# Kernel optimization log

Hardware: AMD Instinct MI355X
Metric: run time of the kernel (lower is better)

The kernel has to match this reference:

```python
import jax, jax.numpy as jnp
import numpy as np

N, K, F_DIM, D = 50000, 20, 256, 128


def setup_inputs() -> dict:
    key = jax.random.key(0)
    ks = jax.random.split(key, 8)
    s = 0.05  # small init scale for numerical stability
    return {
        "h": jax.random.normal(ks[0], (N, F_DIM), dtype=jnp.float32),
        "aggregate_neighbors": jax.random.randint(ks[1], (N, K), 0, N),
        "W_past": jax.random.normal(ks[2], (F_DIM, D), dtype=jnp.float32) * s,
        "W": jax.random.normal(ks[3], (2 * D, D), dtype=jnp.float32) * s,
        "W_ih": jax.random.normal(ks[4], (4 * D, D), dtype=jnp.float32) * s,
        "W_hh": jax.random.normal(ks[5], (4 * D, D), dtype=jnp.float32) * s,
        "b_ih": jax.random.normal(ks[6], (4 * D,), dtype=jnp.float32) * s,
        "b_hh": jax.random.normal(ks[7], (4 * D,), dtype=jnp.float32) * s,
    }


def _lstm(seq, W_ih, W_hh, b_ih, b_hh):
    # seq: (N, K, D) batch_first single-layer LSTM; returns final (h_n, c_n), each (N, D)
    n, _, d = seq.shape

    def step(carry, x_t):
        h_t, c_t = carry
        gates = x_t @ W_ih.T + b_ih + h_t @ W_hh.T + b_hh  # (N, 4D)
        i, f, g, o = jnp.split(gates, 4, axis=-1)
        c = jax.nn.sigmoid(f) * c_t + jax.nn.sigmoid(i) * jnp.tanh(g)
        h_new = jax.nn.sigmoid(o) * jnp.tanh(c)
        return (h_new, c), None

    init = (jnp.zeros((n, d), seq.dtype), jnp.zeros((n, d), seq.dtype))
    (h_n, c_n), _ = jax.lax.scan(step, init, jnp.swapaxes(seq, 0, 1))
    return h_n, c_n


def reference(h, aggregate_neighbors, W_past, W, W_ih, W_hh, b_ih, b_hh):
    hp = h @ W_past                      # (N, D) projected features
    seq = hp[aggregate_neighbors]        # (N, K, D) per-node neighbor gather
    h_n, c_n = _lstm(seq, W_ih, W_hh, b_ih, b_hh)
    neigh = jnp.concatenate([hp, h_n], axis=1)  # (N, 2D)
    out = jax.nn.elu(neigh @ W)          # (N, D)
    return out, h_n, c_n
```

## Files before the change

### kernel.cpp

```cpp
#include <hip/hip_runtime.h>

#define NN 50000
#define KSEQ 20
#define HN_OFF 6400000
#define CN_OFF 12800000

using short8 = __attribute__((ext_vector_type(8))) short;
using f32x4  = __attribute__((ext_vector_type(4))) float;

__device__ __forceinline__ unsigned short f2bf(float f) {
    unsigned int u = __float_as_uint(f);
    return (unsigned short)((u + 0x7FFFu + ((u >> 16) & 1u)) >> 16);
}
__device__ __forceinline__ float exp2x(float x) { float r; asm("v_exp_f32 %0, %1" : "=v"(r) : "v"(x)); return r; }
__device__ __forceinline__ float rcpx(float x)  { float r; asm("v_rcp_f32 %0, %1" : "=v"(r) : "v"(x)); return r; }

#define L2E 1.4426950408889634f
__device__ __forceinline__ float sigp(float y)  { return rcpx(1.f + exp2x(y)); }
__device__ __forceinline__ float tanhp(float y) { return fmaf(-2.f, rcpx(1.f + exp2x(y)), 1.f); }

__global__ void prep_kernel(const float* __restrict__ Wp, const float* __restrict__ W,
                            const float* __restrict__ Wih, const float* __restrict__ Whh,
                            const float* __restrict__ bih, const float* __restrict__ bhh,
                            unsigned short* __restrict__ Wih_b, unsigned short* __restrict__ Whh_b,
                            unsigned short* __restrict__ Wpt, unsigned short* __restrict__ Wtt,
                            float* __restrict__ bsum) {
    int tid = blockIdx.x * blockDim.x + threadIdx.x;
    if (tid < 65536) {
        float sc = ((tid >> 14) == 2) ? (2.f * L2E) : (-L2E);
        Wih_b[tid] = f2bf(Wih[tid] * sc); return;
    }
    tid -= 65536;
    if (tid < 65536) {
        float sc = ((tid >> 14) == 2) ? (2.f * L2E) : (-L2E);
        Whh_b[tid] = f2bf(Whh[tid] * sc); return;
    }
    tid -= 65536;
    if (tid < 32768) { int j = tid >> 8, k = tid & 255; Wpt[tid] = f2bf(Wp[k * 128 + j]); return; }
    tid -= 32768;
    if (tid < 32768) { int j = tid >> 8, k = tid & 255; Wtt[tid] = f2bf(W[k * 128 + j]); return; }
    tid -= 32768;
    if (tid < 512) {
        float sc = ((tid >> 7) == 2) ? (2.f * L2E) : (-L2E);
        bsum[tid] = (bih[tid] + bhh[tid]) * sc;
    }
}

__global__ __launch_bounds__(512, 2) void hp_g_kernel(const float* __restrict__ h,
                                                      const unsigned short* __restrict__ Wpt,
                                                      const unsigned short* __restrict__ Wih_b,
                                                      const float* __restrict__ bsum,
                                                      unsigned short* __restrict__ hp_bf,
                                                      unsigned short* __restrict__ G) {
    __shared__ __align__(16) unsigned char smem[24576];
    const int tid = threadIdx.x;
    const int w = tid >> 6, l = tid & 63;
    const int l15 = l & 15, lq = l >> 4;
    const int base = blockIdx.x * 32;
    const int colj = w * 16 + l15;

#pragma unroll
    for (int i = 0; i < 4; ++i) {
        int chunk = tid + 512 * i;
        int row = chunk >> 6, kc = chunk & 63;
        int grow = base + row;
        float4 v = make_float4(0.f, 0.f, 0.f, 0.f);
        if (grow < NN) v = *(const float4*)(h + (size_t)grow * 256 + kc * 4);
        ushort4 bv = make_ushort4(f2bf(v.x), f2bf(v.y), f2bf(v.z), f2bf(v.w));
        int off = (row * 512 + kc * 8) ^ ((row & 7) << 4);
        *(ushort4*)(smem + off) = bv;
    }
    __syncthreads();

    short8 bf[8];
#pragma unroll
    for (int kt = 0; kt < 8; ++kt)
        bf[kt] = *(const short8*)((const unsigned char*)Wpt + colj * 512 + kt * 64 + lq * 16);

    f32x4 acc[2];
    acc[0] = (f32x4){0.f, 0.f, 0.f, 0.f};
    acc[1] = acc[0];
#pragma unroll
    for (int kt = 0; kt < 8; ++kt) {
#pragma unroll
        for (int rt = 0; rt < 2; ++rt) {
            int arow = rt * 16 + l15;
            int off = (arow * 512 + kt * 64 + lq * 16) ^ ((arow & 7) << 4);
            short8 a = *(const short8*)(smem + off);
            acc[rt] = __builtin_amdgcn_mfma_f32_16x16x32_bf16(a, bf[kt], acc[rt], 0, 0, 0);
        }
    }
#pragma unroll
    for (int rt = 0; rt < 2; ++rt)
#pragma unroll
        for (int r = 0; r < 4; ++r) {
            int row = rt * 16 + lq * 4 + r;
            int grow = base + row;
            unsigned short hb = f2bf(acc[rt][r]);
            if (grow < NN) hp_bf[(size_t)grow * 128 + colj] = hb;
            *(unsigned short*)(smem + 16384 + ((row * 256 + colj * 2) ^ ((row & 7) << 4))) = hb;
        }
    __syncthreads();

    short8 bw4[4][4];
    float bi[4];
#pragma unroll
    for (int g = 0; g < 4; ++g) {
#pragma unroll
        for (int kt = 0; kt < 4; ++kt)
            bw4[g][kt] = *(const short8*)((const unsigned char*)Wih_b + (g * 128 + colj) * 256 + kt * 64 + lq * 16);
        bi[g] = bsum[g * 128 + colj];
    }
    const int off0 = (l15 * 256 + lq * 16) ^ ((l15 & 7) << 4);

    f32x4 ag[4][2];
#pragma unroll
    for (int g = 0; g < 4; ++g) { ag[g][0] = (f32x4){bi[g], bi[g], bi[g], bi[g]}; ag[g][1] = ag[g][0]; }
#pragma unroll
    for (int kt = 0; kt < 4; ++kt)
#pragma unroll
        for (int rt = 0; rt < 2; ++rt) {
            short8 a = *(const short8*)(smem + 16384 + rt * 4096 + (off0 ^ (kt << 6)));
#pragma unroll
            for (int g = 0; g < 4; ++g)
                ag[g][rt] = __builtin_amdgcn_mfma_f32_16x16x32_bf16(a, bw4[g][kt], ag[g][rt], 0, 0, 0);
        }
#pragma unroll
    for (int rt = 0; rt < 2; ++rt)
#pragma unroll
        for (int e = 0; e < 4; ++e) {
            int grow = base + rt * 16 + lq * 4 + e;
            if (grow < NN) {
                ushort4 pk = make_ushort4(f2bf(ag[0][rt][e]), f2bf(ag[1][rt][e]),
                                          f2bf(ag[2][rt][e]), f2bf(ag[3][rt][e]));
                *(ushort4*)(G + (size_t)grow * 512 + colj * 4) = pk;
            }
        }
}

template<int RP>
__device__ __forceinline__ void lstm_step(unsigned char* lds, int t,
    uint2 (&gx)[2][4], const short8 (&bw)[4][4], f32x4& cst,
    const unsigned char* Gp, const unsigned cb,
    const int off0, const int colj, const int lq, const int hwb, const int hswz,
    const int base, float* __restrict__ out)
{
    constexpr int NP = RP ^ 1;
    f32x4 acc[4];
#pragma unroll
    for (int e = 0; e < 4; ++e) {
        uint2 u = gx[RP][e];
        acc[0][e] = __uint_as_float(u.x << 16);
        acc[1][e] = __uint_as_float(u.x & 0xFFFF0000u);
        acc[2][e] = __uint_as_float(u.y << 16);
        acc[3][e] = __uint_as_float(u.y & 0xFFFF0000u);
    }
    if (t > 0) {
        __builtin_amdgcn_s_setprio(1);
#pragma unroll
        for (int kt = 0; kt < 4; ++kt) {
            short8 a = *(const short8*)(lds + RP * 4096 + (off0 ^ (kt << 6)));
#pragma unroll
            for (int g = 0; g < 4; ++g)
                acc[g] = __builtin_amdgcn_mfma_f32_16x16x32_bf16(a, bw[g][kt], acc[g], 0, 0, 0);
        }
        __builtin_amdgcn_s_setprio(0);
    }
    if (t <= 17) {
#pragma unroll
        for (int e = 0; e < 4; ++e) {
            int idx = *(const int*)(lds + 12288 + (lq * 4 + e) * 80 + (t + 2) * 4);
            gx[RP][e] = *(const uint2*)(Gp + (((unsigned)idx << 10) + cb));
        }
    }
#pragma unroll
    for (int e = 0; e < 4; ++e) {
        float c = fmaf(sigp(acc[1][e]), cst[e], sigp(acc[0][e]) * tanhp(acc[2][e]));
        cst[e] = c;
        float hv = sigp(acc[3][e]) * tanhp((2.f * L2E) * c);
        unsigned pk;
        asm("v_cvt_pk_bf16_f32 %0, %1, %2" : "=v"(pk) : "v"(hv), "v"(hv));
        *(unsigned short*)(lds + NP * 4096 + ((hwb + e * 256) ^ (hswz ^ (e << 4)))) = (unsigned short)pk;
        if (t == KSEQ - 1) {
            int grow = base + lq * 4 + e;
            out[HN_OFF + (size_t)grow * 128 + colj] = hv;
            out[CN_OFF + (size_t)grow * 128 + colj] = c;
        }
    }
    __syncthreads();
}

__global__ __launch_bounds__(512, 4) void lstm_kernel(const unsigned short* __restrict__ hp_bf,
                                                      const int* __restrict__ agg,
                                                      const unsigned short* __restrict__ G,
                                                      const unsigned short* __restrict__ Whh_b,
                                                      const unsigned short* __restrict__ Wtt,
                                                      float* __restrict__ out) {
    __shared__ __align__(16) unsigned char lds[14336];
    const int tid = threadIdx.x;
    const int w = tid >> 6, l = tid & 63;
    const int l15 = l & 15, lq = l >> 4;
    const int base = blockIdx.x * 16;
    const int colj = w * 16 + l15;

    if (tid < 256) {
        int row = tid >> 4, c = tid & 15;
        uint4 v = *(const uint4*)((const unsigned char*)hp_bf + (size_t)(base + row) * 256 + c * 16);
        *(uint4*)(lds + 8192 + ((row * 256 + c * 16) ^ ((row & 7) << 4))) = v;
    }
    if (tid < 320) {
        *(int*)(lds + 12288 + tid * 4) = agg[(size_t)base * KSEQ + tid];
    }

    short8 bw[4][4];
#pragma unroll
    for (int g = 0; g < 4; ++g)
#pragma unroll
        for (int kt = 0; kt < 4; ++kt)
            bw[g][kt] = *(const short8*)((const unsigned char*)Whh_b + (g * 128 + colj) * 256 + kt * 64 + lq * 16);

    const int off0 = (l15 * 256 + lq * 16) ^ ((l15 & 7) << 4);
    const int hwb = lq * 1024 + colj * 2;
    const int hswz = (lq & 1) << 6;
    const unsigned char* Gp = (const unsigned char*)G;
    const unsigned cb = (unsigned)colj * 8;

    f32x4 cst = (f32x4){0.f, 0.f, 0.f, 0.f};
    __syncthreads();

    uint2 gx[2][4];
#pragma unroll
    for (int tp = 0; tp < 2; ++tp)
#pragma unroll
        for (int e = 0; e < 4; ++e) {
            int idx = *(const int*)(lds + 12288 + (lq * 4 + e) * 80 + tp * 4);
            gx[tp][e] = *(const uint2*)(Gp + (((unsigned)idx << 10) + cb));
        }

#pragma unroll 1
    for (int tt = 0; tt < KSEQ; tt += 2) {
        lstm_step<0>(lds, tt,     gx, bw, cst, Gp, cb, off0, colj, lq, hwb, hswz, base, out);
        lstm_step<1>(lds, tt + 1, gx, bw, cst, Gp, cb, off0, colj, lq, hwb, hswz, base, out);
    }

    short8 bo[8];
#pragma unroll
    for (int kt = 0; kt < 8; ++kt)
        bo[kt] = *(const short8*)((const unsigned char*)Wtt + colj * 512 + kt * 64 + lq * 16);

    f32x4 a2 = (f32x4){0.f, 0.f, 0.f, 0.f};
#pragma unroll
    for (int kt = 0; kt < 4; ++kt) {
        short8 a = *(const short8*)(lds + 8192 + (off0 ^ (kt << 6)));
        a2 = __builtin_amdgcn_mfma_f32_16x16x32_bf16(a, bo[kt], a2, 0, 0, 0);
    }
#pragma unroll
    for (int kt = 0; kt < 4; ++kt) {
        short8 a = *(const short8*)(lds + (off0 ^ (kt << 6)));
        a2 = __builtin_amdgcn_mfma_f32_16x16x32_bf16(a, bo[kt + 4], a2, 0, 0, 0);
    }
#pragma unroll
    for (int e = 0; e < 4; ++e) {
        int grow = base + lq * 4 + e;
        float v = a2[e];
        out[(size_t)grow * 128 + colj] = (v > 0.f) ? v : (exp2x(L2E * v) - 1.f);
    }
}

extern "C" void kernel_launch(void* const* d_in, const int* in_sizes, int n_in,
                              void* d_out, int out_size, void* d_ws, size_t ws_size,
                              hipStream_t stream) {
    (void)in_sizes; (void)n_in; (void)out_size; (void)ws_size;
    const float* h   = (const float*)d_in[0];
    const int*   agg = (const int*)d_in[1];
    const float* Wp  = (const float*)d_in[2];
    const float* W   = (const float*)d_in[3];
    const float* Wih = (const float*)d_in[4];
    const float* Whh = (const float*)d_in[5];
    const float* bih = (const float*)d_in[6];
    const float* bhh = (const float*)d_in[7];
    float* out = (float*)d_out;

    unsigned short* hp_bf = (unsigned short*)d_ws;
    unsigned short* G     = hp_bf + 6400000;
    unsigned short* Wih_b = G + 25600000;
    unsigned short* Whh_b = Wih_b + 65536;
    unsigned short* Wpt   = Whh_b + 65536;
    unsigned short* Wtt   = Wpt + 32768;
    float*          bsum  = (float*)(Wtt + 32768);

    prep_kernel<<<771, 256, 0, stream>>>(Wp, W, Wih, Whh, bih, bhh, Wih_b, Whh_b, Wpt, Wtt, bsum);
    hp_g_kernel<<<1563, 512, 0, stream>>>(h, Wpt, Wih_b, bsum, hp_bf, G);
    lstm_kernel<<<3125, 512, 0, stream>>>(hp_bf, agg, G, Whh_b, Wtt, out);
}
```

Measured before the change: 300.0 us.

## Single-buffer gate prefetch, transpose index slab, fuse sigmoid/tanh reciprocals

New measurement: 283.4 us. -5.5%, faster.

```diff
diff --git a/kernel.cpp b/kernel.cpp
--- a/kernel.cpp
+++ b/kernel.cpp
@@ -138,23 +138,34 @@
         }
 }
 
+#define SLAB 12288
 template<int RP>
 __device__ __forceinline__ void lstm_step(unsigned char* lds, int t,
-    uint2 (&gx)[2][4], const short8 (&bw)[4][4], f32x4& cst,
+    uint2 (&gx)[4], const short8 (&bw)[4][4], f32x4& cst,
     const unsigned char* Gp, const unsigned cb,
     const int off0, const int colj, const int lq, const int hwb, const int hswz,
     const int base, float* __restrict__ out)
 {
     constexpr int NP = RP ^ 1;
+    int4 idx4;
+    if (t < KSEQ - 1)
+        idx4 = *(const int4*)(lds + SLAB + (t + 1) * 64 + lq * 16);
+
     f32x4 acc[4];
 #pragma unroll
     for (int e = 0; e < 4; ++e) {
-        uint2 u = gx[RP][e];
+        uint2 u = gx[e];
         acc[0][e] = __uint_as_float(u.x << 16);
         acc[1][e] = __uint_as_float(u.x & 0xFFFF0000u);
         acc[2][e] = __uint_as_float(u.y << 16);
         acc[3][e] = __uint_as_float(u.y & 0xFFFF0000u);
     }
+    if (t < KSEQ - 1) {
+        gx[0] = *(const uint2*)(Gp + (((unsigned)idx4.x << 10) + cb));
+        gx[1] = *(const uint2*)(Gp + (((unsigned)idx4.y << 10) + cb));
+        gx[2] = *(const uint2*)(Gp + (((unsigned)idx4.z << 10) + cb));
+        gx[3] = *(const uint2*)(Gp + (((unsigned)idx4.w << 10) + cb));
+    }
     if (t > 0) {
         __builtin_amdgcn_s_setprio(1);
 #pragma unroll
@@ -166,18 +177,17 @@
         }
         __builtin_amdgcn_s_setprio(0);
     }
-    if (t <= 17) {
-#pragma unroll
-        for (int e = 0; e < 4; ++e) {
-            int idx = *(const int*)(lds + 12288 + (lq * 4 + e) * 80 + (t + 2) * 4);
-            gx[RP][e] = *(const uint2*)(Gp + (((unsigned)idx << 10) + cb));
-        }
-    }
 #pragma unroll
     for (int e = 0; e < 4; ++e) {
-        float c = fmaf(sigp(acc[1][e]), cst[e], sigp(acc[0][e]) * tanhp(acc[2][e]));
+        float Ai = 1.f + exp2x(acc[0][e]);
+        float Af = 1.f + exp2x(acc[1][e]);
+        float B  = 1.f + exp2x(acc[2][e]);
+        float AiB = Ai * B;
+        float c = fmaf(cst[e], AiB, Af * (B - 2.f)) * rcpx(Af * AiB);
         cst[e] = c;
-        float hv = sigp(acc[3][e]) * tanhp((2.f * L2E) * c);
+        float C  = 1.f + exp2x((2.f * L2E) * c);
+        float Do = 1.f + exp2x(acc[3][e]);
+        float hv = (C - 2.f) * rcpx(C * Do);
         unsigned pk;
         asm("v_cvt_pk_bf16_f32 %0, %1, %2" : "=v"(pk) : "v"(hv), "v"(hv));
         *(unsigned short*)(lds + NP * 4096 + ((hwb + e * 256) ^ (hswz ^ (e << 4)))) = (unsigned short)pk;
@@ -209,7 +219,8 @@
         *(uint4*)(lds + 8192 + ((row * 256 + c * 16) ^ ((row & 7) << 4))) = v;
     }
     if (tid < 320) {
-        *(int*)(lds + 12288 + tid * 4) = agg[(size_t)base * KSEQ + tid];
+        int row = tid / 20, t = tid - row * 20;
+        *(int*)(lds + SLAB + t * 64 + row * 4) = agg[(size_t)base * KSEQ + tid];
     }
 
     short8 bw[4][4];
@@ -228,14 +239,14 @@
     f32x4 cst = (f32x4){0.f, 0.f, 0.f, 0.f};
     __syncthreads();
 
-    uint2 gx[2][4];
-#pragma unroll
-    for (int tp = 0; tp < 2; ++tp)
-#pragma unroll
-        for (int e = 0; e < 4; ++e) {
-            int idx = *(const int*)(lds + 12288 + (lq * 4 + e) * 80 + tp * 4);
-            gx[tp][e] = *(const uint2*)(Gp + (((unsigned)idx << 10) + cb));
-        }
+    uint2 gx[4];
+    {
+        int4 i4 = *(const int4*)(lds + SLAB + lq * 16);
+        gx[0] = *(const uint2*)(Gp + (((unsigned)i4.x << 10) + cb));
+        gx[1] = *(const uint2*)(Gp + (((unsigned)i4.y << 10) + cb));
+        gx[2] = *(const uint2*)(Gp + (((unsigned)i4.z << 10) + cb));
+        gx[3] = *(const uint2*)(Gp + (((unsigned)i4.w << 10) + cb));
+    }
 
 #pragma unroll 1
     for (int tt = 0; tt < KSEQ; tt += 2) {
```
